# Performance work log

Hardware: AMD Instinct MI355X
Metric: run time of the kernel (lower is better)

## Reference

```python
import jax, jax.numpy as jnp
import numpy as np

B, S, E, H = 4, 1024, 512, 8
DK = E // H


def setup_inputs() -> dict:
    key = jax.random.key(0)
    ks = jax.random.split(key, 16)
    s = 1.0 / np.sqrt(E)
    inp = {
        "query": jax.random.normal(ks[0], (B, S, E), dtype=jnp.float32),
        "key": jax.random.normal(ks[1], (B, S, E), dtype=jnp.float32),
        "value": jax.random.normal(ks[2], (B, S, E), dtype=jnp.float32),
        "dist_conv": jax.random.uniform(ks[3], (B, S, S), dtype=jnp.float32),
        "mask": jax.random.randint(ks[4], (B, S, S), 0, 2, dtype=jnp.int32),
        # four Linear(E, E) layers: q, k, v, out (torch: y = x @ W.T + b)
        "Wq": jax.random.normal(ks[5], (E, E), dtype=jnp.float32) * s,
        "bq": jnp.zeros((E,), dtype=jnp.float32),
        "Wk": jax.random.normal(ks[6], (E, E), dtype=jnp.float32) * s,
        "bk": jnp.zeros((E,), dtype=jnp.float32),
        "Wv": jax.random.normal(ks[7], (E, E), dtype=jnp.float32) * s,
        "bv": jnp.zeros((E,), dtype=jnp.float32),
        "Wo": jax.random.normal(ks[8], (E, E), dtype=jnp.float32) * s,
        "bo": jnp.zeros((E,), dtype=jnp.float32),
        # 1x1 Conv2d(1, H) -> ReLU -> 1x1 Conv2d(H, H)
        "cw1": jax.random.normal(ks[9], (H,), dtype=jnp.float32),  # [out_c] (in_c=1, k=1)
        "cb1": jnp.zeros((H,), dtype=jnp.float32),
        "cw2": jax.random.normal(ks[10], (H, H), dtype=jnp.float32) * (1.0 / np.sqrt(H)),
        "cb2": jnp.zeros((H,), dtype=jnp.float32),
    }
    return inp


def reference(query, key, value, dist_conv, mask, Wq, bq, Wk, bk, Wv, bv, Wo, bo, cw1, cb1, cw2, cb2):
    # projections, split into heads: [B, H, S, DK]
    def proj(x, W, b):
        y = jnp.einsum("bse,fe->bsf", x, W) + b
        return y.reshape(B, S, H, DK).transpose(0, 2, 1, 3)

    q = proj(query, Wq, bq)
    k = proj(key, Wk, bk)
    v = proj(value, Wv, bv)

    # 1x1 conv stack on distance matrix: [B,S,S] -> [B,H,S,S]
    t = jax.nn.relu(dist_conv[:, None] * cw1[None, :, None, None] + cb1[None, :, None, None])
    bias = jnp.einsum("bhij,gh->bgij", t, cw2) + cb2[None, :, None, None]

    scores = jnp.einsum("bhqd,bhkd->bhqk", q, k) / jnp.sqrt(jnp.float32(DK))
    scores = scores * bias
    scores = jnp.where(mask[:, None] == 0, jnp.float32(-1e9), scores)
    p_attn = jax.nn.softmax(scores, axis=-1)

    x = jnp.einsum("bhqk,bhkd->bhqd", p_attn, v)
    x = x.transpose(0, 2, 1, 3).reshape(B, S, E)
    return jnp.einsum("bse,fe->bsf", x, Wo) + bo
```

## Files before the change

### kernel.cpp

```cpp
#include <hip/hip_runtime.h>
#include <hip/hip_bf16.h>
#include <math.h>

#define B_ 4
#define S_ 1024
#define E_ 512
#define H_ 8
#define DK_ 64

typedef short bf16x8 __attribute__((ext_vector_type(8)));
typedef float f32x4 __attribute__((ext_vector_type(4)));

#define MFMA16(a, b, c) __builtin_amdgcn_mfma_f32_16x16x32_bf16((a), (b), (c), 0, 0, 0)
#define cfence() asm volatile("" ::: "memory")

__device__ __forceinline__ void gl_lds16(const void* gptr, void* lptr) {
    __builtin_amdgcn_global_load_lds(
        (const __attribute__((address_space(1))) unsigned int*)gptr,
        (__attribute__((address_space(3))) unsigned int*)lptr,
        16, 0, 0);
}

__device__ __forceinline__ unsigned short bf16_bits(float v) {
    __hip_bfloat16 h = __float2bfloat16(v);
    return *(unsigned short*)&h;
}

__global__ __launch_bounds__(256) void convert_bf16(
    const float* __restrict__ q, const float* __restrict__ k, const float* __restrict__ v,
    const float* __restrict__ wq, const float* __restrict__ wk,
    const float* __restrict__ wv, const float* __restrict__ wo,
    __hip_bfloat16* qc, __hip_bfloat16* kc, __hip_bfloat16* vc,
    __hip_bfloat16* wqc, __hip_bfloat16* wkc, __hip_bfloat16* wvc, __hip_bfloat16* woc) {
    const int blk = blockIdx.x;
    const float* src;
    __hip_bfloat16* dst;
    int base;
    if (blk < 1024)      { src = q; dst = qc; base = blk; }
    else if (blk < 2048) { src = k; dst = kc; base = blk - 1024; }
    else if (blk < 3072) { src = v; dst = vc; base = blk - 2048; }
    else {
        const int wz = (blk - 3072) >> 7;
        base = (blk - 3072) & 127;
        switch (wz) {
            case 0: src = wq; dst = wqc; break;
            case 1: src = wk; dst = wkc; break;
            case 2: src = wv; dst = wvc; break;
            default: src = wo; dst = woc; break;
        }
    }
    const int idx = (base * 256 + threadIdx.x) * 8;
    float4 a = *(const float4*)(src + idx);
    float4 bb = *(const float4*)(src + idx + 4);
    union { __hip_bfloat16 h[8]; uint4 u; } o;
    o.h[0] = __float2bfloat16(a.x);  o.h[1] = __float2bfloat16(a.y);
    o.h[2] = __float2bfloat16(a.z);  o.h[3] = __float2bfloat16(a.w);
    o.h[4] = __float2bfloat16(bb.x); o.h[5] = __float2bfloat16(bb.y);
    o.h[6] = __float2bfloat16(bb.z); o.h[7] = __float2bfloat16(bb.w);
    *(uint4*)(dst + idx) = o.u;
}

__global__ __launch_bounds__(256) void bias_pre(
    const float* __restrict__ dist, const int* __restrict__ mask,
    const float* __restrict__ cw1, const float* __restrict__ cb1,
    const float* __restrict__ cw2, const float* __restrict__ cb2,
    __hip_bfloat16* __restrict__ biasS) {
    const int bi = blockIdx.x;
    const int b = bi >> 10, i = bi & 1023;
    const int j0 = threadIdx.x * 4;
    const size_t dbase = ((size_t)b * 1024 + i) * 1024 + j0;
    float4 d4 = *(const float4*)(dist + dbase);
    int4 m4 = *(const int4*)(mask + dbase);
    float dv[4] = {d4.x, d4.y, d4.z, d4.w};
    int mv[4] = {m4.x, m4.y, m4.z, m4.w};
    float tt[4][8];
#pragma unroll
    for (int e = 0; e < 4; ++e)
#pragma unroll
        for (int h = 0; h < 8; ++h)
            tt[e][h] = fmaxf(fmaf(dv[e], cw1[h], cb1[h]), 0.f);
#pragma unroll
    for (int g = 0; g < 8; ++g) {
        const float c2 = cb2[g];
        union { unsigned short us[4]; uint2 u2; } o;
#pragma unroll
        for (int e = 0; e < 4; ++e) {
            float bv = c2;
#pragma unroll
            for (int h = 0; h < 8; ++h) bv = fmaf(tt[e][h], cw2[g * 8 + h], bv);
            unsigned short u = bf16_bits(bv * 0.125f);
            if (mv[e] == 0) u = 0xFF80u;
            o.us[e] = u;
        }
        *(uint2*)(biasS + ((size_t)(b * 8 + g) * 1024 + i) * 1024 + j0) = o.u2;
    }
}

__device__ __forceinline__ void gemm_core(const __hip_bfloat16* A, const __hip_bfloat16* W,
                                          char* sA, char* sW, int m0, int n0,
                                          f32x4 acc[4][2]) {
    const int t = threadIdx.x;
    const int w = t >> 6, lane = t & 63;
    const int wm = (w >> 1) * 64, wn = (w & 1) * 32;
    const int g = lane >> 4, ln = lane & 15;

    for (int kc = 0; kc < 8; ++kc) {
        __syncthreads();
#pragma unroll
        for (int i = 0; i < 4; ++i) {
            int L = (i * 4 + w) * 64 + lane;
            int r = L >> 3, cs = L & 7;
            int c = cs ^ (r & 7);
            gl_lds16((const char*)A + (size_t)(m0 + r) * 1024 + kc * 128 + c * 16,
                     sA + (i * 4 + w) * 1024);
        }
#pragma unroll
        for (int i = 0; i < 2; ++i) {
            int L = (i * 4 + w) * 64 + lane;
            int r = L >> 3, cs = L & 7;
            int c = cs ^ (r & 7);
            gl_lds16((const char*)W + (size_t)(n0 + r) * 1024 + kc * 128 + c * 16,
                     sW + (i * 4 + w) * 1024);
        }
        __syncthreads();
#pragma unroll
        for (int ks = 0; ks < 2; ++ks) {
            bf16x8 af[4], bf[2];
#pragma unroll
            for (int mt = 0; mt < 4; ++mt) {
                int m = wm + mt * 16 + ln;
                int c = ks * 4 + g;
                af[mt] = *(const bf16x8*)(sA + m * 128 + (c ^ (m & 7)) * 16);
            }
#pragma unroll
            for (int nt = 0; nt < 2; ++nt) {
                int n = wn + nt * 16 + ln;
                int c = ks * 4 + g;
                bf[nt] = *(const bf16x8*)(sW + n * 128 + (c ^ (n & 7)) * 16);
            }
#pragma unroll
            for (int mt = 0; mt < 4; ++mt)
#pragma unroll
                for (int nt = 0; nt < 2; ++nt)
                    acc[mt][nt] = MFMA16(af[mt], bf[nt], acc[mt][nt]);
        }
    }
}

__global__ __launch_bounds__(256) void proj_gemm(
    const __hip_bfloat16* __restrict__ qc, const __hip_bfloat16* __restrict__ kc,
    const __hip_bfloat16* __restrict__ vc,
    const __hip_bfloat16* __restrict__ wqc, const __hip_bfloat16* __restrict__ wkc,
    const __hip_bfloat16* __restrict__ wvc,
    const float* __restrict__ bq, const float* __restrict__ bk, const float* __restrict__ bv,
    __hip_bfloat16* qbh, __hip_bfloat16* kbh, __hip_bfloat16* vt) {
    __shared__ char smem[24576];
    char* sA = smem;
    char* sW = smem + 16384;
    const int z = blockIdx.z;
    const __hip_bfloat16* A;
    const __hip_bfloat16* W;
    const float* bias;
    __hip_bfloat16* dst;
    if (z == 0)      { A = qc; W = wqc; bias = bq; dst = qbh; }
    else if (z == 1) { A = kc; W = wkc; bias = bk; dst = kbh; }
    else             { A = vc; W = wvc; bias = bv; dst = vt; }

    const int m0 = blockIdx.y * 128, n0 = blockIdx.x * 64;
    f32x4 acc[4][2] = {};
    gemm_core(A, W, sA, sW, m0, n0, acc);
    __syncthreads();

    const int t = threadIdx.x;
    const int w = t >> 6, lane = t & 63;
    const int wm = (w >> 1) * 64, wn = (w & 1) * 32;
    const int g = lane >> 4, ln = lane & 15;
    const int b = m0 >> 10;
    const int hh = n0 >> 6;
    float bv2[2];
#pragma unroll
    for (int nt = 0; nt < 2; ++nt) bv2[nt] = bias[n0 + wn + nt * 16 + ln];

    __hip_bfloat16* T = (__hip_bfloat16*)smem;
    if (z != 2) {
#pragma unroll
        for (int mt = 0; mt < 4; ++mt)
#pragma unroll
            for (int nt = 0; nt < 2; ++nt)
#pragma unroll
                for (int r = 0; r < 4; ++r) {
                    int lm = wm + mt * 16 + g * 4 + r;
                    int n = wn + nt * 16 + ln;
                    T[lm * 72 + n] = __float2bfloat16(acc[mt][nt][r] + bv2[nt]);
                }
        __syncthreads();
        const int lm = t >> 1, half = t & 1;
        const char* srow = smem + lm * 144 + half * 64;
        char* gdst = (char*)dst +
                     (((size_t)(b * 8 + hh) * 1024 + (m0 & 1023) + lm) * 64) * 2 + half * 64;
#pragma unroll
        for (int j = 0; j < 4; ++j)
            *(uint4*)(gdst + j * 16) = *(const uint4*)(srow + j * 16);
    } else {
#pragma unroll
        for (int mt = 0; mt < 4; ++mt)
#pragma unroll
            for (int nt = 0; nt < 2; ++nt)
#pragma unroll
                for (int r = 0; r < 4; ++r) {
                    int lm = wm + mt * 16 + g * 4 + r;
                    int n = wn + nt * 16 + ln;
                    T[lm * 66 + n] = __float2bfloat16(acc[mt][nt][r] + bv2[nt]);
                }
        __syncthreads();
        const int dk = t >> 2, a = t & 3;
        union { __hip_bfloat16 h[32]; uint4 u[4]; } P;
#pragma unroll
        for (int i = 0; i < 32; ++i)
            P.h[i] = T[(a * 32 + i) * 66 + dk];
        char* gdst = (char*)vt +
                     (((size_t)(b * 8 + hh) * 64 + dk) * 1024 + (m0 & 1023) + a * 32) * 2;
#pragma unroll
        for (int j = 0; j < 4; ++j)
            *(uint4*)(gdst + j * 16) = P.u[j];
    }
}

__global__ __launch_bounds__(256) void out_gemm(
    const __hip_bfloat16* __restrict__ X, const __hip_bfloat16* __restrict__ woc,
    const float* __restrict__ bo, float* __restrict__ out) {
    __shared__ char smem[24576];
    char* sA = smem;
    char* sW = smem + 16384;
    const int m0 = blockIdx.y * 128, n0 = blockIdx.x * 64;
    f32x4 acc[4][2] = {};
    gemm_core(X, woc, sA, sW, m0, n0, acc);

    const int t = threadIdx.x;
    const int w = t >> 6, lane = t & 63;
    const int wm = (w >> 1) * 64, wn = (w & 1) * 32;
    const int g = lane >> 4, ln = lane & 15;
    float bv2[2];
#pragma unroll
    for (int nt = 0; nt < 2; ++nt) bv2[nt] = bo[n0 + wn + nt * 16 + ln];
#pragma unroll
    for (int mt = 0; mt < 4; ++mt)
#pragma unroll
        for (int nt = 0; nt < 2; ++nt)
#pragma unroll
            for (int r = 0; r < 4; ++r) {
                int m = m0 + wm + mt * 16 + g * 4 + r;
                int f = n0 + wn + nt * 16 + ln;
                out[(size_t)m * 512 + f] = acc[mt][nt][r] + bv2[nt];
            }
}

__global__ __launch_bounds__(256) void attn(
    const __hip_bfloat16* __restrict__ Qb, const __hip_bfloat16* __restrict__ Kb,
    const __hip_bfloat16* __restrict__ Vt, const __hip_bfloat16* __restrict__ biasS,
    __hip_bfloat16* __restrict__ X) {
    __shared__ char sK[8192];
    __shared__ char sV[8192];
    __shared__ char sScP[4][4352];
    __shared__ float sBr[4][16];

    const int t = threadIdx.x, w = t >> 6, lane = t & 63;
    const int g = lane >> 4, ln = lane & 15;
    const int qr = lane >> 2, a = lane & 3;
    const int bh = blockIdx.y;
    const int q0 = blockIdx.x * 64;

    float* sc = (float*)(sScP[w]);
    __hip_bfloat16* sp = (__hip_bfloat16*)(sScP[w]);

    bf16x8 qf[2];
    {
        const char* qbase = (const char*)Qb + ((size_t)bh * 1024 + q0 + w * 16 + ln) * 128;
        qf[0] = *(const bf16x8*)(qbase + g * 16);
        qf[1] = *(const bf16x8*)(qbase + 64 + g * 16);
    }

    float m_st = -1e30f, l_st = 0.f;
    f32x4 O[4] = {};

    const size_t kbase = (size_t)bh * 1024 * 128;
    const size_t vbase = (size_t)bh * 64 * 2048;
    const __hip_bfloat16* brow = biasS + ((size_t)bh * 1024 + q0 + w * 16 + qr) * 1024;

    for (int kt = 0; kt < S_; kt += 64) {
        __syncthreads();
#pragma unroll
        for (int i = 0; i < 2; ++i) {
            int L = (i * 4 + w) * 64 + lane;
            int r = L >> 3, cs = L & 7;
            int c = cs ^ (r & 7);
            gl_lds16((const char*)Kb + kbase + (size_t)(kt + r) * 128 + c * 16,
                     sK + (i * 4 + w) * 1024);
            gl_lds16((const char*)Vt + vbase + (size_t)r * 2048 + (size_t)kt * 2 + c * 16,
                     sV + (i * 4 + w) * 1024);
        }
        union { uint4 u[2]; unsigned short us[16]; } bb;
        bb.u[0] = *(const uint4*)(brow + kt + a * 16);
        bb.u[1] = *(const uint4*)(brow + kt + a * 16 + 8);
        __syncthreads();

        f32x4 scv[4] = {};
#pragma unroll
        for (int tt = 0; tt < 4; ++tt)
#pragma unroll
            for (int ks = 0; ks < 2; ++ks) {
                int key = tt * 16 + ln;
                int c = ks * 4 + g;
                bf16x8 kf = *(const bf16x8*)(sK + key * 128 + (c ^ (key & 7)) * 16);
                scv[tt] = MFMA16(qf[ks], kf, scv[tt]);
            }

        cfence();
#pragma unroll
        for (int tt = 0; tt < 4; ++tt)
#pragma unroll
            for (int r = 0; r < 4; ++r)
                sc[(g * 4 + r) * 66 + tt * 16 + ln] = scv[tt][r];
        cfence();

        float sr[16];
        {
            const float* scrow = sc + qr * 66 + a * 16;
#pragma unroll
            for (int j = 0; j < 8; ++j) {
                float2 v2 = *(const float2*)(scrow + j * 2);
                sr[j * 2] = v2.x; sr[j * 2 + 1] = v2.y;
            }
        }
        cfence();

        float mx = -1e30f;
#pragma unroll
        for (int e = 0; e < 16; ++e) {
            unsigned int bits = bb.us[e];
            float f = __uint_as_float(bits << 16);
            float s = sr[e] * f;
            s = (bits == 0xFF80u) ? -1e9f : s;
            sr[e] = s;
            mx = fmaxf(mx, s);
        }
        mx = fmaxf(mx, __shfl_xor(mx, 1));
        mx = fmaxf(mx, __shfl_xor(mx, 2));
        const float mnew = fmaxf(m_st, mx);
        const float alpha = __expf(m_st - mnew);
        m_st = mnew;
        float rs = 0.f;
        union { __hip_bfloat16 hh16[16]; uint4 u[2]; } Pk;
#pragma unroll
        for (int i = 0; i < 16; ++i) {
            float p = __expf(sr[i] - mnew);
            rs += p;
            Pk.hh16[i] = __float2bfloat16(p);
        }
        rs += __shfl_xor(rs, 1);
        rs += __shfl_xor(rs, 2);
        l_st = l_st * alpha + rs;

        *(uint4*)(sp + qr * 72 + a * 16) = Pk.u[0];
        *(uint4*)(sp + qr * 72 + a * 16 + 8) = Pk.u[1];
        cfence();

        if (a == 0) sBr[w][qr] = alpha;
        float al4[4];
#pragma unroll
        for (int r = 0; r < 4; ++r) al4[r] = sBr[w][g * 4 + r];
#pragma unroll
        for (int tt = 0; tt < 4; ++tt)
#pragma unroll
            for (int r = 0; r < 4; ++r) O[tt][r] *= al4[r];

#pragma unroll
        for (int ks = 0; ks < 2; ++ks) {
            bf16x8 pf = *(const bf16x8*)(sp + ln * 72 + ks * 32 + g * 8);
#pragma unroll
            for (int tt = 0; tt < 4; ++tt) {
                int dk = tt * 16 + ln;
                int c = ks * 4 + g;
                bf16x8 vf = *(const bf16x8*)(sV + dk * 128 + (c ^ (dk & 7)) * 16);
                O[tt] = MFMA16(pf, vf, O[tt]);
            }
        }
        cfence();
    }

    if (a == 0) sBr[w][qr] = l_st;
    __builtin_amdgcn_s_waitcnt(0);
    const int b = bh >> 3, h = bh & 7;
#pragma unroll
    for (int r = 0; r < 4; ++r) {
        float inv = 1.f / sBr[w][g * 4 + r];
        int q = q0 + w * 16 + g * 4 + r;
#pragma unroll
        for (int tt = 0; tt < 4; ++tt) {
            int dk = tt * 16 + ln;
            X[((size_t)(b * 1024 + q)) * 512 + h * 64 + dk] = __float2bfloat16(O[tt][r] * inv);
        }
    }
}

extern "C" void kernel_launch(void* const* d_in, const int* in_sizes, int n_in,
                              void* d_out, int out_size, void* d_ws, size_t ws_size,
                              hipStream_t stream) {
    (void)in_sizes; (void)n_in; (void)out_size; (void)ws_size;
    const float* query = (const float*)d_in[0];
    const float* key   = (const float*)d_in[1];
    const float* value = (const float*)d_in[2];
    const float* dist  = (const float*)d_in[3];
    const int*   mask  = (const int*)d_in[4];
    const float* Wq = (const float*)d_in[5];
    const float* bq = (const float*)d_in[6];
    const float* Wk = (const float*)d_in[7];
    const float* bk = (const float*)d_in[8];
    const float* Wv = (const float*)d_in[9];
    const float* bv = (const float*)d_in[10];
    const float* Wo = (const float*)d_in[11];
    const float* bo = (const float*)d_in[12];
    const float* cw1 = (const float*)d_in[13];
    const float* cb1 = (const float*)d_in[14];
    const float* cw2 = (const float*)d_in[15];
    const float* cb2 = (const float*)d_in[16];
    float* out = (float*)d_out;

    char* ws = (char*)d_ws;
    const size_t MB = 1 << 20;
    __hip_bfloat16* qc  = (__hip_bfloat16*)(ws + 0 * MB);
    __hip_bfloat16* kc  = (__hip_bfloat16*)(ws + 4 * MB);
    __hip_bfloat16* vc  = (__hip_bfloat16*)(ws + 8 * MB);
    __hip_bfloat16* wqc = (__hip_bfloat16*)(ws + 12 * MB);
    __hip_bfloat16* wkc = (__hip_bfloat16*)(ws + 12 * MB + 512 * 1024);
    __hip_bfloat16* wvc = (__hip_bfloat16*)(ws + 13 * MB);
    __hip_bfloat16* woc = (__hip_bfloat16*)(ws + 13 * MB + 512 * 1024);
    __hip_bfloat16* qbh = (__hip_bfloat16*)(ws + 14 * MB);
    __hip_bfloat16* kbh = (__hip_bfloat16*)(ws + 18 * MB);
    __hip_bfloat16* vt  = (__hip_bfloat16*)(ws + 22 * MB);
    __hip_bfloat16* x   = (__hip_bfloat16*)(ws + 26 * MB);
    __hip_bfloat16* bS  = (__hip_bfloat16*)(ws + 32 * MB);

    hipLaunchKernelGGL(convert_bf16, dim3(3584), dim3(256), 0, stream,
                       query, key, value, Wq, Wk, Wv, Wo,
                       qc, kc, vc, wqc, wkc, wvc, woc);
    hipLaunchKernelGGL(bias_pre, dim3(4096), dim3(256), 0, stream,
                       dist, mask, cw1, cb1, cw2, cb2, bS);
    hipLaunchKernelGGL(proj_gemm, dim3(8, 32, 3), dim3(256), 0, stream,
                       qc, kc, vc, wqc, wkc, wvc, bq, bk, bv, qbh, kbh, vt);
    hipLaunchKernelGGL(attn, dim3(16, 32), dim3(256), 0, stream,
                       qbh, kbh, vt, bS, x);
    hipLaunchKernelGGL(out_gemm, dim3(8, 32), dim3(256), 0, stream,
                       x, woc, bo, out);
}
```

Baseline: 200.7 us.

## Merge prep kernels, widen GEMM K-chunks and N tiles, double attention key tile

The bf16 conversion and bias precompute kernels are fused into one launch. The GEMM core now loads 128-wide K chunks with a 16-way XOR swizzle, and the projection GEMM uses 128x128 tiles with a two-pass epilogue. The attention kernel stages 128 keys per barrier and runs two 64-key softmax phases inside. Together these cut launches, barriers and loop iterations, at the cost of much larger LDS use per block, which can lower occupancy.

```diff
diff --git a/kernel.cpp b/kernel.cpp
--- a/kernel.cpp
+++ b/kernel.cpp
@@ -26,13 +26,49 @@
     return *(unsigned short*)&h;
 }
 
-__global__ __launch_bounds__(256) void convert_bf16(
+__global__ __launch_bounds__(256) void prep(
     const float* __restrict__ q, const float* __restrict__ k, const float* __restrict__ v,
     const float* __restrict__ wq, const float* __restrict__ wk,
     const float* __restrict__ wv, const float* __restrict__ wo,
+    const float* __restrict__ dist, const int* __restrict__ mask,
+    const float* __restrict__ cw1, const float* __restrict__ cb1,
+    const float* __restrict__ cw2, const float* __restrict__ cb2,
     __hip_bfloat16* qc, __hip_bfloat16* kc, __hip_bfloat16* vc,
-    __hip_bfloat16* wqc, __hip_bfloat16* wkc, __hip_bfloat16* wvc, __hip_bfloat16* woc) {
+    __hip_bfloat16* wqc, __hip_bfloat16* wkc, __hip_bfloat16* wvc, __hip_bfloat16* woc,
+    __hip_bfloat16* __restrict__ biasS) {
     const int blk = blockIdx.x;
+    if (blk >= 3584) {
+        const int bi = blk - 3584;
+        const int b = bi >> 10, i = bi & 1023;
+        const int j0 = threadIdx.x * 4;
+        const size_t dbase = ((size_t)b * 1024 + i) * 1024 + j0;
+        float4 d4 = *(const float4*)(dist + dbase);
+        int4 m4 = *(const int4*)(mask + dbase);
+        float dv[4] = {d4.x, d4.y, d4.z, d4.w};
+        int mv[4] = {m4.x, m4.y, m4.z, m4.w};
+        float tt[4][8];
+#pragma unroll
+        for (int e = 0; e < 4; ++e)
+#pragma unroll
+            for (int h = 0; h < 8; ++h)
+                tt[e][h] = fmaxf(fmaf(dv[e], cw1[h], cb1[h]), 0.f);
+#pragma unroll
+        for (int g = 0; g < 8; ++g) {
+            const float c2 = cb2[g];
+            union { unsigned short us[4]; uint2 u2; } o;
+#pragma unroll
+            for (int e = 0; e < 4; ++e) {
+                float bv = c2;
+#pragma unroll
+                for (int h = 0; h < 8; ++h) bv = fmaf(tt[e][h], cw2[g * 8 + h], bv);
+                unsigned short u = bf16_bits(bv * 0.125f);
+                if (mv[e] == 0) u = 0xFF80u;
+                o.us[e] = u;
+            }
+            *(uint2*)(biasS + ((size_t)(b * 8 + g) * 1024 + i) * 1024 + j0) = o.u2;
+        }
+        return;
+    }
     const float* src;
     __hip_bfloat16* dst;
     int base;
@@ -60,88 +96,53 @@
     *(uint4*)(dst + idx) = o.u;
 }
 
-__global__ __launch_bounds__(256) void bias_pre(
-    const float* __restrict__ dist, const int* __restrict__ mask,
-    const float* __restrict__ cw1, const float* __restrict__ cb1,
-    const float* __restrict__ cw2, const float* __restrict__ cb2,
-    __hip_bfloat16* __restrict__ biasS) {
-    const int bi = blockIdx.x;
-    const int b = bi >> 10, i = bi & 1023;
-    const int j0 = threadIdx.x * 4;
-    const size_t dbase = ((size_t)b * 1024 + i) * 1024 + j0;
-    float4 d4 = *(const float4*)(dist + dbase);
-    int4 m4 = *(const int4*)(mask + dbase);
-    float dv[4] = {d4.x, d4.y, d4.z, d4.w};
-    int mv[4] = {m4.x, m4.y, m4.z, m4.w};
-    float tt[4][8];
-#pragma unroll
-    for (int e = 0; e < 4; ++e)
-#pragma unroll
-        for (int h = 0; h < 8; ++h)
-            tt[e][h] = fmaxf(fmaf(dv[e], cw1[h], cb1[h]), 0.f);
-#pragma unroll
-    for (int g = 0; g < 8; ++g) {
-        const float c2 = cb2[g];
-        union { unsigned short us[4]; uint2 u2; } o;
-#pragma unroll
-        for (int e = 0; e < 4; ++e) {
-            float bv = c2;
-#pragma unroll
-            for (int h = 0; h < 8; ++h) bv = fmaf(tt[e][h], cw2[g * 8 + h], bv);
-            unsigned short u = bf16_bits(bv * 0.125f);
-            if (mv[e] == 0) u = 0xFF80u;
-            o.us[e] = u;
-        }
-        *(uint2*)(biasS + ((size_t)(b * 8 + g) * 1024 + i) * 1024 + j0) = o.u2;
-    }
-}
-
-__device__ __forceinline__ void gemm_core(const __hip_bfloat16* A, const __hip_bfloat16* W,
-                                          char* sA, char* sW, int m0, int n0,
-                                          f32x4 acc[4][2]) {
+template <int NROWS_W, int NT>
+__device__ __forceinline__ void gemm_core128(const __hip_bfloat16* A, const __hip_bfloat16* W,
+                                             char* sA, char* sW, int m0, int n0,
+                                             f32x4 acc[4][NT]) {
     const int t = threadIdx.x;
     const int w = t >> 6, lane = t & 63;
-    const int wm = (w >> 1) * 64, wn = (w & 1) * 32;
+    const int wm = (w >> 1) * 64, wn = (w & 1) * (NT * 16);
     const int g = lane >> 4, ln = lane & 15;
 
-    for (int kc = 0; kc < 8; ++kc) {
+    for (int kc = 0; kc < 4; ++kc) {
         __syncthreads();
 #pragma unroll
-        for (int i = 0; i < 4; ++i) {
+        for (int i = 0; i < 8; ++i) {
             int L = (i * 4 + w) * 64 + lane;
-            int r = L >> 3, cs = L & 7;
-            int c = cs ^ (r & 7);
-            gl_lds16((const char*)A + (size_t)(m0 + r) * 1024 + kc * 128 + c * 16,
+            int r = L >> 4, cs = L & 15;
+            int c = cs ^ (r & 15);
+            gl_lds16((const char*)A + (size_t)(m0 + r) * 1024 + kc * 256 + c * 16,
                      sA + (i * 4 + w) * 1024);
         }
 #pragma unroll
-        for (int i = 0; i < 2; ++i) {
+        for (int i = 0; i < NROWS_W / 16; ++i) {
             int L = (i * 4 + w) * 64 + lane;
-            int r = L >> 3, cs = L & 7;
-            int c = cs ^ (r & 7);
-            gl_lds16((const char*)W + (size_t)(n0 + r) * 1024 + kc * 128 + c * 16,
+            int r = L >> 4, cs = L & 15;
+            int c = cs ^ (r & 15);
+            gl_lds16((const char*)W + (size_t)(n0 + r) * 1024 + kc * 256 + c * 16,
                      sW + (i * 4 + w) * 1024);
         }
         __syncthreads();
 #pragma unroll
-        for (int ks = 0; ks < 2; ++ks) {
-            bf16x8 af[4], bf[2];
+        for (int ks = 0; ks < 4; ++ks) {
+            bf16x8 af[4], bf[NT];
 #pragma unroll
             for (int mt = 0; mt < 4; ++mt) {
                 int m = wm + mt * 16 + ln;
                 int c = ks * 4 + g;
-                af[mt] = *(const bf16x8*)(sA + m * 128 + (c ^ (m & 7)) * 16);
-            }
-#pragma unroll
-            for (int nt = 0; nt < 2; ++nt) {
+                af[mt] = *(const bf16x8*)(sA + m * 256 + (c ^ (m & 15)) * 16);
+            }
+#pragma unroll
+            for (int nt = 0; nt < NT; ++nt) {
                 int n = wn + nt * 16 + ln;
                 int c = ks * 4 + g;
-                bf[nt] = *(const bf16x8*)(sW + n * 128 + (c ^ (n & 7)) * 16);
+                bf[nt] = *(const bf16x8*)(sW + n * 256 + (c ^ (n & 15)) * 16);
             }
 #pragma unroll
             for (int mt = 0; mt < 4; ++mt)
 #pragma unroll
-                for (int nt = 0; nt < 2; ++nt)
+                for (int nt = 0; nt < NT; ++nt)
                     acc[mt][nt] = MFMA16(af[mt], bf[nt], acc[mt][nt]);
         }
     }
@@ -154,9 +155,9 @@
     const __hip_bfloat16* __restrict__ wvc,
     const float* __restrict__ bq, const float* __restrict__ bk, const float* __restrict__ bv,
     __hip_bfloat16* qbh, __hip_bfloat16* kbh, __hip_bfloat16* vt) {
-    __shared__ char smem[24576];
+    __shared__ char smem[65536];
     char* sA = smem;
-    char* sW = smem + 16384;
+    char* sW = smem + 32768;
     const int z = blockIdx.z;
     const __hip_bfloat16* A;
     const __hip_bfloat16* W;
@@ -166,75 +167,85 @@
     else if (z == 1) { A = kc; W = wkc; bias = bk; dst = kbh; }
     else             { A = vc; W = wvc; bias = bv; dst = vt; }
 
-    const int m0 = blockIdx.y * 128, n0 = blockIdx.x * 64;
-    f32x4 acc[4][2] = {};
-    gemm_core(A, W, sA, sW, m0, n0, acc);
+    const int m0 = blockIdx.y * 128, n0 = blockIdx.x * 128;
+    f32x4 acc[4][4] = {};
+    gemm_core128<128, 4>(A, W, sA, sW, m0, n0, acc);
     __syncthreads();
 
     const int t = threadIdx.x;
     const int w = t >> 6, lane = t & 63;
-    const int wm = (w >> 1) * 64, wn = (w & 1) * 32;
+    const int wm = (w >> 1) * 64, wn = (w & 1) * 64;
     const int g = lane >> 4, ln = lane & 15;
     const int b = m0 >> 10;
-    const int hh = n0 >> 6;
-    float bv2[2];
-#pragma unroll
-    for (int nt = 0; nt < 2; ++nt) bv2[nt] = bias[n0 + wn + nt * 16 + ln];
+    float bv4[4];
+#pragma unroll
+    for (int nt = 0; nt < 4; ++nt) bv4[nt] = bias[n0 + wn + nt * 16 + ln];
 
     __hip_bfloat16* T = (__hip_bfloat16*)smem;
     if (z != 2) {
 #pragma unroll
-        for (int mt = 0; mt < 4; ++mt)
-#pragma unroll
-            for (int nt = 0; nt < 2; ++nt)
-#pragma unroll
-                for (int r = 0; r < 4; ++r) {
-                    int lm = wm + mt * 16 + g * 4 + r;
-                    int n = wn + nt * 16 + ln;
-                    T[lm * 72 + n] = __float2bfloat16(acc[mt][nt][r] + bv2[nt]);
-                }
-        __syncthreads();
-        const int lm = t >> 1, half = t & 1;
-        const char* srow = smem + lm * 144 + half * 64;
-        char* gdst = (char*)dst +
-                     (((size_t)(b * 8 + hh) * 1024 + (m0 & 1023) + lm) * 64) * 2 + half * 64;
-#pragma unroll
-        for (int j = 0; j < 4; ++j)
-            *(uint4*)(gdst + j * 16) = *(const uint4*)(srow + j * 16);
+        for (int p = 0; p < 2; ++p) {
+            if (wm == p * 64) {
+#pragma unroll
+                for (int mt = 0; mt < 4; ++mt)
+#pragma unroll
+                    for (int nt = 0; nt < 4; ++nt)
+#pragma unroll
+                        for (int r = 0; r < 4; ++r)
+                            T[(mt * 16 + g * 4 + r) * 136 + wn + nt * 16 + ln] =
+                                __float2bfloat16(acc[mt][nt][r] + bv4[nt]);
+            }
+            __syncthreads();
+            const int lr = t >> 2, quarter = t & 3;
+            const char* srow = (const char*)T + lr * 272 + quarter * 64;
+            const int s = (m0 & 1023) + p * 64 + lr;
+            const int h = (n0 >> 6) + (quarter >> 1);
+            char* gdst = (char*)dst +
+                         (((size_t)(b * 8 + h) * 1024 + s) * 64 + (quarter & 1) * 32) * 2;
+#pragma unroll
+            for (int j = 0; j < 4; ++j)
+                *(uint4*)(gdst + j * 16) = *(const uint4*)(srow + j * 16);
+            __syncthreads();
+        }
     } else {
 #pragma unroll
-        for (int mt = 0; mt < 4; ++mt)
-#pragma unroll
-            for (int nt = 0; nt < 2; ++nt)
-#pragma unroll
-                for (int r = 0; r < 4; ++r) {
-                    int lm = wm + mt * 16 + g * 4 + r;
-                    int n = wn + nt * 16 + ln;
-                    T[lm * 66 + n] = __float2bfloat16(acc[mt][nt][r] + bv2[nt]);
-                }
-        __syncthreads();
-        const int dk = t >> 2, a = t & 3;
-        union { __hip_bfloat16 h[32]; uint4 u[4]; } P;
-#pragma unroll
-        for (int i = 0; i < 32; ++i)
-            P.h[i] = T[(a * 32 + i) * 66 + dk];
-        char* gdst = (char*)vt +
-                     (((size_t)(b * 8 + hh) * 64 + dk) * 1024 + (m0 & 1023) + a * 32) * 2;
-#pragma unroll
-        for (int j = 0; j < 4; ++j)
-            *(uint4*)(gdst + j * 16) = P.u[j];
+        for (int p = 0; p < 2; ++p) {
+            if (wm == p * 64) {
+#pragma unroll
+                for (int mt = 0; mt < 4; ++mt)
+#pragma unroll
+                    for (int nt = 0; nt < 4; ++nt)
+#pragma unroll
+                        for (int r = 0; r < 4; ++r)
+                            T[(mt * 16 + g * 4 + r) * 130 + wn + nt * 16 + ln] =
+                                __float2bfloat16(acc[mt][nt][r] + bv4[nt]);
+            }
+            __syncthreads();
+            const int c = t >> 1, sel = t & 1;
+            union { __hip_bfloat16 h[32]; uint4 u[4]; } P;
+#pragma unroll
+            for (int i = 0; i < 32; ++i)
+                P.h[i] = T[(sel * 32 + i) * 130 + c];
+            const int h = (n0 >> 6) + (c >> 6), dk = c & 63;
+            char* gdst = (char*)vt +
+                         (((size_t)(b * 8 + h) * 64 + dk) * 1024 + (m0 & 1023) + p * 64 + sel * 32) * 2;
+#pragma unroll
+            for (int j = 0; j < 4; ++j)
+                *(uint4*)(gdst + j * 16) = P.u[j];
+            __syncthreads();
+        }
     }
 }
 
 __global__ __launch_bounds__(256) void out_gemm(
     const __hip_bfloat16* __restrict__ X, const __hip_bfloat16* __restrict__ woc,
     const float* __restrict__ bo, float* __restrict__ out) {
-    __shared__ char smem[24576];
+    __shared__ char smem[49152];
     char* sA = smem;
-    char* sW = smem + 16384;
+    char* sW = smem + 32768;
     const int m0 = blockIdx.y * 128, n0 = blockIdx.x * 64;
     f32x4 acc[4][2] = {};
-    gemm_core(X, woc, sA, sW, m0, n0, acc);
+    gemm_core128<64, 2>(X, woc, sA, sW, m0, n0, acc);
 
     const int t = threadIdx.x;
     const int w = t >> 6, lane = t & 63;
@@ -259,8 +270,8 @@
     const __hip_bfloat16* __restrict__ Qb, const __hip_bfloat16* __restrict__ Kb,
     const __hip_bfloat16* __restrict__ Vt, const __hip_bfloat16* __restrict__ biasS,
     __hip_bfloat16* __restrict__ X) {
-    __shared__ char sK[8192];
-    __shared__ char sV[8192];
+    __shared__ char sK[16384];
+    __shared__ char sV[16384];
     __shared__ char sScP[4][4352];
     __shared__ float sBr[4][16];
 
@@ -287,105 +298,117 @@
     const size_t vbase = (size_t)bh * 64 * 2048;
     const __hip_bfloat16* brow = biasS + ((size_t)bh * 1024 + q0 + w * 16 + qr) * 1024;
 
-    for (int kt = 0; kt < S_; kt += 64) {
+    for (int kt = 0; kt < S_; kt += 128) {
         __syncthreads();
 #pragma unroll
-        for (int i = 0; i < 2; ++i) {
+        for (int i = 0; i < 4; ++i) {
             int L = (i * 4 + w) * 64 + lane;
             int r = L >> 3, cs = L & 7;
             int c = cs ^ (r & 7);
             gl_lds16((const char*)Kb + kbase + (size_t)(kt + r) * 128 + c * 16,
                      sK + (i * 4 + w) * 1024);
+        }
+#pragma unroll
+        for (int i = 0; i < 4; ++i) {
+            int L = (i * 4 + w) * 64 + lane;
+            int r = L >> 4, cs = L & 15;
+            int c = cs ^ (r & 15);
             gl_lds16((const char*)Vt + vbase + (size_t)r * 2048 + (size_t)kt * 2 + c * 16,
                      sV + (i * 4 + w) * 1024);
         }
-        union { uint4 u[2]; unsigned short us[16]; } bb;
-        bb.u[0] = *(const uint4*)(brow + kt + a * 16);
-        bb.u[1] = *(const uint4*)(brow + kt + a * 16 + 8);
+        union { uint4 u[2]; unsigned short us[16]; } bb[2];
+#pragma unroll
+        for (int ph = 0; ph < 2; ++ph) {
+            bb[ph].u[0] = *(const uint4*)(brow + kt + ph * 64 + a * 16);
+            bb[ph].u[1] = *(const uint4*)(brow + kt + ph * 64 + a * 16 + 8);
+        }
         __syncthreads();
 
-        f32x4 scv[4] = {};
-#pragma unroll
-        for (int tt = 0; tt < 4; ++tt)
+#pragma unroll
+        for (int ph = 0; ph < 2; ++ph) {
+            f32x4 scv[4] = {};
+#pragma unroll
+            for (int tt = 0; tt < 4; ++tt)
+#pragma unroll
+                for (int ks = 0; ks < 2; ++ks) {
+                    int key = ph * 64 + tt * 16 + ln;
+                    int c = ks * 4 + g;
+                    bf16x8 kf = *(const bf16x8*)(sK + key * 128 + (c ^ (key & 7)) * 16);
+                    scv[tt] = MFMA16(qf[ks], kf, scv[tt]);
+                }
+
+            cfence();
+#pragma unroll
+            for (int tt = 0; tt < 4; ++tt)
+#pragma unroll
+                for (int r = 0; r < 4; ++r)
+                    sc[(g * 4 + r) * 66 + tt * 16 + ln] = scv[tt][r];
+            cfence();
+
+            float sr[16];
+            {
+                const float* scrow = sc + qr * 66 + a * 16;
+#pragma unroll
+                for (int j = 0; j < 8; ++j) {
+                    float2 v2 = *(const float2*)(scrow + j * 2);
+                    sr[j * 2] = v2.x; sr[j * 2 + 1] = v2.y;
+                }
+            }
+            cfence();
+
+            float mx = -1e30f;
+#pragma unroll
+            for (int e = 0; e < 16; ++e) {
+                unsigned int bits = bb[ph].us[e];
+                float f = __uint_as_float(bits << 16);
+                float s = sr[e] * f;
+                s = (bits == 0xFF80u) ? -1e9f : s;
+                sr[e] = s;
+                mx = fmaxf(mx, s);
+            }
+            mx = fmaxf(mx, __shfl_xor(mx, 1));
+            mx = fmaxf(mx, __shfl_xor(mx, 2));
+            const float mnew = fmaxf(m_st, mx);
+            const float alpha = __expf(m_st - mnew);
+            m_st = mnew;
+            float rs = 0.f;
+            union { __hip_bfloat16 hh16[16]; uint4 u[2]; } Pk;
+#pragma unroll
+            for (int i = 0; i < 16; ++i) {
+                float p = __expf(sr[i] - mnew);
+                rs += p;
+                Pk.hh16[i] = __float2bfloat16(p);
+            }
+            rs += __shfl_xor(rs, 1);
+            rs += __shfl_xor(rs, 2);
+            l_st = l_st * alpha + rs;
+
+            *(uint4*)(sp + qr * 72 + a * 16) = Pk.u[0];
+            *(uint4*)(sp + qr * 72 + a * 16 + 8) = Pk.u[1];
+            cfence();
+
+            if (a == 0) sBr[w][qr] = alpha;
+            float al4[4];
+#pragma unroll
+            for (int r = 0; r < 4; ++r) al4[r] = sBr[w][g * 4 + r];
+#pragma unroll
+            for (int tt = 0; tt < 4; ++tt)
+#pragma unroll
+                for (int r = 0; r < 4; ++r) O[tt][r] *= al4[r];
+
 #pragma unroll
             for (int ks = 0; ks < 2; ++ks) {
-                int key = tt * 16 + ln;
-                int c = ks * 4 + g;
-                bf16x8 kf = *(const bf16x8*)(sK + key * 128 + (c ^ (key & 7)) * 16);
-                scv[tt] = MFMA16(qf[ks], kf, scv[tt]);
-            }
-
-        cfence();
-#pragma unroll
-        for (int tt = 0; tt < 4; ++tt)
-#pragma unroll
-            for (int r = 0; r < 4; ++r)
-                sc[(g * 4 + r) * 66 + tt * 16 + ln] = scv[tt][r];
-        cfence();
-
-        float sr[16];
-        {
-            const float* scrow = sc + qr * 66 + a * 16;
-#pragma unroll
-            for (int j = 0; j < 8; ++j) {
-                float2 v2 = *(const float2*)(scrow + j * 2);
-                sr[j * 2] = v2.x; sr[j * 2 + 1] = v2.y;
-            }
-        }
-        cfence();
-
-        float mx = -1e30f;
-#pragma unroll
-        for (int e = 0; e < 16; ++e) {
-            unsigned int bits = bb.us[e];
-            float f = __uint_as_float(bits << 16);
-            float s = sr[e] * f;
-            s = (bits == 0xFF80u) ? -1e9f : s;
-            sr[e] = s;
-            mx = fmaxf(mx, s);
-        }
-        mx = fmaxf(mx, __shfl_xor(mx, 1));
-        mx = fmaxf(mx, __shfl_xor(mx, 2));
-        const float mnew = fmaxf(m_st, mx);
-        const float alpha = __expf(m_st - mnew);
-        m_st = mnew;
-        float rs = 0.f;
-        union { __hip_bfloat16 hh16[16]; uint4 u[2]; } Pk;
-#pragma unroll
-        for (int i = 0; i < 16; ++i) {
-            float p = __expf(sr[i] - mnew);
-            rs += p;
-            Pk.hh16[i] = __float2bfloat16(p);
-        }
-        rs += __shfl_xor(rs, 1);
-        rs += __shfl_xor(rs, 2);
-        l_st = l_st * alpha + rs;
-
-        *(uint4*)(sp + qr * 72 + a * 16) = Pk.u[0];
-        *(uint4*)(sp + qr * 72 + a * 16 + 8) = Pk.u[1];
-        cfence();
-
-        if (a == 0) sBr[w][qr] = alpha;
-        float al4[4];
-#pragma unroll
-        for (int r = 0; r < 4; ++r) al4[r] = sBr[w][g * 4 + r];
-#pragma unroll
-        for (int tt = 0; tt < 4; ++tt)
-#pragma unroll
-            for (int r = 0; r < 4; ++r) O[tt][r] *= al4[r];
-
-#pragma unroll
-        for (int ks = 0; ks < 2; ++ks) {
-            bf16x8 pf = *(const bf16x8*)(sp + ln * 72 + ks * 32 + g * 8);
-#pragma unroll
-            for (int tt = 0; tt < 4; ++tt) {
-                int dk = tt * 16 + ln;
-                int c = ks * 4 + g;
-                bf16x8 vf = *(const bf16x8*)(sV + dk * 128 + (c ^ (dk & 7)) * 16);
-                O[tt] = MFMA16(pf, vf, O[tt]);
-            }
-        }
-        cfence();
+                bf16x8 pf = *(const bf16x8*)(sp + ln * 72 + ks * 32 + g * 8);
+#pragma unroll
+                for (int tt = 0; tt < 4; ++tt) {
+                    int dk = tt * 16 + ln;
+                    int ck = ph * 8 + ks * 4 + g;
+                    bf16x8 vf = *(const bf16x8*)(sV + dk * 256 + (ck ^ (dk & 15)) * 16);
+                    O[tt] = MFMA16(pf, vf, O[tt]);
+                }
+            }
+            cfence();
+        }
     }
 
     if (a == 0) sBr[w][qr] = l_st;
@@ -441,12 +464,11 @@
     __hip_bfloat16* x   = (__hip_bfloat16*)(ws + 26 * MB);
     __hip_bfloat16* bS  = (__hip_bfloat16*)(ws + 32 * MB);
 
-    hipLaunchKernelGGL(convert_bf16, dim3(3584), dim3(256), 0, stream,
-                       query, key, value, Wq, Wk, Wv, Wo,
-                       qc, kc, vc, wqc, wkc, wvc, woc);
-    hipLaunchKernelGGL(bias_pre, dim3(4096), dim3(256), 0, stream,
-                       dist, mask, cw1, cb1, cw2, cb2, bS);
-    hipLaunchKernelGGL(proj_gemm, dim3(8, 32, 3), dim3(256), 0, stream,
+    hipLaunchKernelGGL(prep, dim3(7680), dim3(256), 0, stream,
+                       query, key, value, Wq, Wk, Wv, Wo, dist, mask,
+                       cw1, cb1, cw2, cb2,
+                       qc, kc, vc, wqc, wkc, wvc, woc, bS);
+    hipLaunchKernelGGL(proj_gemm, dim3(4, 32, 3), dim3(256), 0, stream,
                        qc, kc, vc, wqc, wkc, wvc, bq, bk, bv, qbh, kbh, vt);
     hipLaunchKernelGGL(attn, dim3(16, 32), dim3(256), 0, stream,
                        qbh, kbh, vt, bS, x);
```

Result: no change. 197.8 us (-1.4%).
